# Kernel optimization log

Measured on AMD Instinct MI355X. Metric: run time of the kernel, lower is better.

## Reference

```python
import jax, jax.numpy as jnp
import numpy as np

T, B, XD, H, F = 1024, 256, 64, 256, 256  # seq_len, batch, x_dim, dim_RNN, feature dims
ALPHAS = [0.001, 0.01, 0.1]


def _alphas_per_unit():
    a = np.sort(np.asarray(ALPHAS, dtype=np.float32))
    assign = np.array([a[i % len(a)] for i in range(H)], dtype=np.float32)
    return jnp.asarray(np.sort(assign))  # [H]


def setup_inputs() -> dict:
    key = jax.random.key(0)
    ks = jax.random.split(key, 16)

    def w(k, shape, fan_in):
        return jax.random.normal(k, shape, jnp.float32) / np.sqrt(fan_in).astype(np.float32)

    return {
        "x": jax.random.normal(ks[0], (T, B, XD), jnp.float32),
        # feature_extractor_x: Linear(XD->F), Linear(F->F), tanh after each
        "Wx0": w(ks[1], (F, XD), XD), "bx0": jnp.zeros((F,), jnp.float32),
        "Wx1": w(ks[2], (F, F), F),   "bx1": jnp.zeros((F,), jnp.float32),
        # nn.RNN(F, H): tanh cell
        "Wih": w(ks[3], (H, F), F), "Whh": w(ks[4], (H, H), H),
        "bih": jnp.zeros((H,), jnp.float32), "bhh": jnp.zeros((H,), jnp.float32),
        # mlp_h_x: Linear(H->F), Linear(F->F), tanh after each
        "Wh0": w(ks[5], (F, H), H), "bh0": jnp.zeros((F,), jnp.float32),
        "Wh1": w(ks[6], (F, F), F), "bh1": jnp.zeros((F,), jnp.float32),
        # gen_out: Linear(F->XD)
        "Wg": w(ks[7], (XD, F), F), "bg": jnp.zeros((XD,), jnp.float32),
    }


def reference(x, Wx0, bx0, Wx1, bx1, Wih, Whh, bih, bhh, Wh0, bh0, Wh1, bh1, Wg, bg):
    act = jnp.tanh
    alphas = _alphas_per_unit()  # [H]

    # feature extractor applied to all timesteps at once (non-autonomous path)
    feat = act(jnp.einsum('tbx,fx->tbf', x, Wx0) + bx0)
    feat = act(jnp.einsum('tbf,gf->tbg', feat, Wx1) + bx1)  # [T,B,F]

    def step(h, ft):
        # y_t is generated from h BEFORE the recurrence update
        d = act(h @ Wh0.T + bh0)
        d = act(d @ Wh1.T + bh1)
        y = d @ Wg.T + bg  # [B,XD]
        h_raw = jnp.tanh(ft @ Wih.T + bih + h @ Whh.T + bhh)
        h_new = (1.0 - alphas) * h + alphas * h_raw  # leaky alpha-blend
        return h_new, y

    h0 = jnp.zeros((B, H), x.dtype)
    _, y = jax.lax.scan(step, h0, feat)  # y: [T,B,XD]
    return y
```

## Files before the change

### kernel.cpp

```cpp
#include <hip/hip_runtime.h>
#include <cstddef>


typedef _Float16 halfx8 __attribute__((ext_vector_type(8)));
typedef _Float16 halfx4 __attribute__((ext_vector_type(4)));
typedef float    f32x4  __attribute__((ext_vector_type(4)));

#define T_LEN 1024
#define B_SZ  256
#define H_DIM 256
#define M_ROWS (T_LEN * B_SZ)

__device__ __forceinline__ float fast_tanh(float x) {
  float e = __expf(2.0f * x);
  return 1.0f - 2.0f / (e + 1.0f);
}

__device__ __forceinline__ float alpha_of(int j) {
  return (j < 86) ? 0.001f : ((j < 171) ? 0.01f : 0.1f);
}

__device__ __forceinline__ void lds_barrier() {
  asm volatile("s_waitcnt lgkmcnt(0)\n\ts_barrier" ::: "memory");
}

template <int KCH, bool TANH, bool INF32, bool ZXT>
__global__ __launch_bounds__(512, 2)
void gemm8(const void* __restrict__ Ap, const float* __restrict__ W,
           const float* __restrict__ bias, void* __restrict__ Cp, int mtiles) {
  constexpr int K  = KCH * 32;
  constexpr int KP = K + 8;
  __shared__ __attribute__((aligned(16))) _Float16 Ah[32][KP];

  const int tid  = threadIdx.x;
  const int lane = tid & 63;
  const int wave = tid >> 6;
  const int l15  = lane & 15;
  const int quad = lane >> 4;
  const int jw   = wave * 32;

  halfx8 Bf[2][KCH];
  float  bcol[2];
  int    jj[2];
#pragma unroll
  for (int nt = 0; nt < 2; nt++) {
    jj[nt]   = jw + nt * 16 + l15;
    bcol[nt] = bias[jj[nt]];
#pragma unroll
    for (int ks = 0; ks < KCH; ks++) {
      const float* wp = W + (size_t)jj[nt] * K + ks * 32 + quad * 8;
      float4 w0 = *(const float4*)wp;
      float4 w1 = *(const float4*)(wp + 4);
      halfx8 f;
      f[0] = (_Float16)w0.x; f[1] = (_Float16)w0.y;
      f[2] = (_Float16)w0.z; f[3] = (_Float16)w0.w;
      f[4] = (_Float16)w1.x; f[5] = (_Float16)w1.y;
      f[6] = (_Float16)w1.z; f[7] = (_Float16)w1.w;
      Bf[nt][ks] = f;
    }
  }

  const int srow = tid >> 4;
  const int sk4  = tid & 15;

  for (int bm = blockIdx.x; bm < mtiles; bm += gridDim.x) {
    if constexpr (INF32) {
      const float* A = (const float*)Ap + (size_t)bm * 32 * K;
      constexpr int SEG = K / 64;
      float4 tv[SEG];
#pragma unroll
      for (int s = 0; s < SEG; s++)
        tv[s] = *(const float4*)(A + (size_t)srow * K + (sk4 + s * 16) * 4);
#pragma unroll
      for (int s = 0; s < SEG; s++) {
        halfx4 h;
        h[0] = (_Float16)tv[s].x; h[1] = (_Float16)tv[s].y;
        h[2] = (_Float16)tv[s].z; h[3] = (_Float16)tv[s].w;
        *(halfx4*)&Ah[srow][(sk4 + s * 16) * 4] = h;
      }
    } else {
      const _Float16* A = (const _Float16*)Ap + (size_t)bm * 32 * K;
      constexpr int SEG = K / 128;
      halfx8 tv[SEG];
#pragma unroll
      for (int s = 0; s < SEG; s++)
        tv[s] = *(const halfx8*)(A + (size_t)srow * K + (sk4 + s * 16) * 8);
#pragma unroll
      for (int s = 0; s < SEG; s++)
        *(halfx8*)&Ah[srow][(sk4 + s * 16) * 8] = tv[s];
    }
    lds_barrier();

    f32x4 acc[2][2];
#pragma unroll
    for (int mi = 0; mi < 2; mi++)
#pragma unroll
      for (int nt = 0; nt < 2; nt++) acc[mi][nt] = (f32x4){0.f, 0.f, 0.f, 0.f};

#pragma unroll
    for (int ks = 0; ks < KCH; ks++)
#pragma unroll
      for (int mi = 0; mi < 2; mi++) {
        halfx8 a = *(const halfx8*)&Ah[mi * 16 + l15][ks * 32 + quad * 8];
#pragma unroll
        for (int nt = 0; nt < 2; nt++)
          acc[mi][nt] = __builtin_amdgcn_mfma_f32_16x16x32_f16(a, Bf[nt][ks], acc[mi][nt], 0, 0, 0);
      }

    if constexpr (ZXT) {
      _Float16* C = (_Float16*)Cp;
      const size_t tb = (size_t)(bm >> 3) * (H_DIM * B_SZ) + (bm & 7) * 32 + quad * 4;
#pragma unroll
      for (int mi = 0; mi < 2; mi++)
#pragma unroll
        for (int nt = 0; nt < 2; nt++) {
          halfx4 o;
#pragma unroll
          for (int rg = 0; rg < 4; rg++)
            o[rg] = (_Float16)(acc[mi][nt][rg] + bcol[nt]);
          *(halfx4*)(C + tb + (size_t)jj[nt] * B_SZ + mi * 16) = o;
        }
    } else {
      _Float16* C = (_Float16*)Cp;
#pragma unroll
      for (int mi = 0; mi < 2; mi++)
#pragma unroll
        for (int nt = 0; nt < 2; nt++)
#pragma unroll
          for (int rg = 0; rg < 4; rg++) {
            const int rowg = bm * 32 + mi * 16 + quad * 4 + rg;
            float v = acc[mi][nt][rg] + bcol[nt];
            if (TANH) v = fast_tanh(v);
            C[(size_t)rowg * 256 + jj[nt]] = (_Float16)v;
          }
    }
    lds_barrier();
  }
}

__global__ __launch_bounds__(256, 2)
void gemm4_out(const _Float16* __restrict__ A, const float* __restrict__ W,
               const float* __restrict__ bias, float* __restrict__ C,
               int mtiles) {
  constexpr int K = 256, KCH = 8, KP = 264;
  __shared__ __attribute__((aligned(16))) _Float16 Ah[32][KP];

  const int tid  = threadIdx.x;
  const int lane = tid & 63;
  const int wave = tid >> 6;
  const int l15  = lane & 15;
  const int quad = lane >> 4;
  const int jcol = wave * 16 + l15;

  halfx8 Bf[KCH];
  const float bc = bias[jcol];
#pragma unroll
  for (int ks = 0; ks < KCH; ks++) {
    const float* wp = W + (size_t)jcol * K + ks * 32 + quad * 8;
    float4 w0 = *(const float4*)wp;
    float4 w1 = *(const float4*)(wp + 4);
    halfx8 f;
    f[0] = (_Float16)w0.x; f[1] = (_Float16)w0.y;
    f[2] = (_Float16)w0.z; f[3] = (_Float16)w0.w;
    f[4] = (_Float16)w1.x; f[5] = (_Float16)w1.y;
    f[6] = (_Float16)w1.z; f[7] = (_Float16)w1.w;
    Bf[ks] = f;
  }

  const int srow = tid >> 3;
  const int sk   = tid & 7;

  for (int bm = blockIdx.x; bm < mtiles; bm += gridDim.x) {
    const _Float16* Ab = A + (size_t)bm * 32 * K;
    halfx8 tv[4];
#pragma unroll
    for (int s = 0; s < 4; s++)
      tv[s] = *(const halfx8*)(Ab + (size_t)srow * K + (sk + s * 8) * 8);
#pragma unroll
    for (int s = 0; s < 4; s++)
      *(halfx8*)&Ah[srow][(sk + s * 8) * 8] = tv[s];
    lds_barrier();

    f32x4 acc[2];
#pragma unroll
    for (int mi = 0; mi < 2; mi++) acc[mi] = (f32x4){0.f, 0.f, 0.f, 0.f};
#pragma unroll
    for (int ks = 0; ks < KCH; ks++)
#pragma unroll
      for (int mi = 0; mi < 2; mi++) {
        halfx8 a = *(const halfx8*)&Ah[mi * 16 + l15][ks * 32 + quad * 8];
        acc[mi] = __builtin_amdgcn_mfma_f32_16x16x32_f16(a, Bf[ks], acc[mi], 0, 0, 0);
      }

#pragma unroll
    for (int mi = 0; mi < 2; mi++)
#pragma unroll
      for (int rg = 0; rg < 4; rg++) {
        const int rowg = bm * 32 + mi * 16 + quad * 4 + rg;
        C[(size_t)rowg * 64 + jcol] = acc[mi][rg] + bc;
      }
    lds_barrier();
  }
}

__global__ __launch_bounds__(1024, 4)
void rnn_serial(const _Float16* __restrict__ zxT,
                _Float16* __restrict__ h_all,
                const float* __restrict__ Whh,
                const float* __restrict__ bhh_p)
{
  __shared__ __attribute__((aligned(16))) _Float16 hB[2][16][264];

  const int tid  = threadIdx.x;
  const int lane = tid & 63;
  const int wave = tid >> 6;
  const int l15  = lane & 15;
  const int quad = lane >> 4;
  const int r0   = blockIdx.x * 16;
  const int jcol = wave * 16 + l15;

  halfx8 Bf[8];
#pragma unroll
  for (int ks = 0; ks < 8; ks++) {
    const float* wp = Whh + (size_t)jcol * H_DIM + ks * 32 + quad * 8;
    float4 w0 = *(const float4*)wp;
    float4 w1 = *(const float4*)(wp + 4);
    halfx8 f;
    f[0] = (_Float16)w0.x; f[1] = (_Float16)w0.y;
    f[2] = (_Float16)w0.z; f[3] = (_Float16)w0.w;
    f[4] = (_Float16)w1.x; f[5] = (_Float16)w1.y;
    f[6] = (_Float16)w1.z; f[7] = (_Float16)w1.w;
    Bf[ks] = f;
  }
  const float bj  = bhh_p[jcol];
  const float aj  = alpha_of(jcol);
  const float oma = 1.0f - aj;

  for (int i = tid; i < 16 * 264; i += 1024) (&hB[0][0][0])[i] = (_Float16)0.0f;
  __syncthreads();

  const _Float16* rdp[2] = {&hB[0][l15][quad * 8], &hB[1][l15][quad * 8]};
  _Float16*       wrp[2] = {&hB[1][quad * 4][jcol], &hB[0][quad * 4][jcol]};

  const _Float16* zp = zxT + (size_t)jcol * B_SZ + r0 + quad * 4;
  _Float16*       hp = h_all + (size_t)(r0 + quad * 4) * H_DIM + jcol;
  constexpr int STRIDE = B_SZ * H_DIM;

  float  zc[4];
  halfx4 zA;
  {
    halfx4 z0 = *(const halfx4*)zp;
    zA = *(const halfx4*)(zp + STRIDE);
    zp += 2 * (size_t)STRIDE;
#pragma unroll
    for (int rg = 0; rg < 4; rg++) zc[rg] = (float)z0[rg];
  }

  float    hreg[4] = {0.f, 0.f, 0.f, 0.f};
  _Float16 hh[4]   = {(_Float16)0.f, (_Float16)0.f, (_Float16)0.f, (_Float16)0.f};

  auto step = [&](int p) {
    halfx4 znew = *(const halfx4*)zp;
    zp += STRIDE;

    f32x4 acc = {0.f, 0.f, 0.f, 0.f};
    const _Float16* rd = rdp[p];
#pragma unroll
    for (int ks = 0; ks < 8; ks++) {
      halfx8 a = *(const halfx8*)(rd + ks * 32);
      acc = __builtin_amdgcn_mfma_f32_16x16x32_f16(a, Bf[ks], acc, 0, 0, 0);
    }

    _Float16* wr = wrp[p];
#pragma unroll
    for (int rg = 0; rg < 4; rg++) {
      float ho = hreg[rg];
      float hr = fast_tanh(zc[rg] + acc[rg] + bj);
      float hn = oma * ho + aj * hr;
      hp[rg * H_DIM] = hh[rg];
      hreg[rg] = hn;
      _Float16 hf = (_Float16)hn;
      hh[rg] = hf;
      wr[rg * 264] = hf;
    }
    hp += STRIDE;

    lds_barrier();

#pragma unroll
    for (int rg = 0; rg < 4; rg++) zc[rg] = (float)zA[rg];
    zA = znew;
  };

  for (int it = 0; it < T_LEN / 2; ++it) {
    step(0);
    step(1);
  }
}

extern "C" void kernel_launch(void* const* d_in, const int* in_sizes, int n_in,
                              void* d_out, int out_size, void* d_ws, size_t ws_size,
                              hipStream_t stream) {
  const float* x   = (const float*)d_in[0];
  const float* Wx0 = (const float*)d_in[1];
  const float* bx0 = (const float*)d_in[2];
  const float* Wx1 = (const float*)d_in[3];
  const float* bx1 = (const float*)d_in[4];
  const float* Wih = (const float*)d_in[5];
  const float* Whh = (const float*)d_in[6];
  const float* bih = (const float*)d_in[7];
  const float* bhh = (const float*)d_in[8];
  const float* Wh0 = (const float*)d_in[9];
  const float* bh0 = (const float*)d_in[10];
  const float* Wh1 = (const float*)d_in[11];
  const float* bh1 = (const float*)d_in[12];
  const float* Wg  = (const float*)d_in[13];
  const float* bg  = (const float*)d_in[14];
  float* out = (float*)d_out;

  _Float16* bufA = (_Float16*)d_ws;
  _Float16* bufB = bufA + (size_t)M_ROWS * 256;

  const int MT = M_ROWS / 32;

  gemm8<2, true, true, false><<<512, 512, 0, stream>>>(x, Wx0, bx0, bufA, MT);
  gemm8<8, true, false, false><<<512, 512, 0, stream>>>(bufA, Wx1, bx1, bufB, MT);
  gemm8<8, false, false, true><<<512, 512, 0, stream>>>(bufB, Wih, bih, bufA, MT);
  rnn_serial<<<16, 1024, 0, stream>>>(bufA, bufB, Whh, bhh);
  gemm8<8, true, false, false><<<512, 512, 0, stream>>>(bufB, Wh0, bh0, bufA, MT);
  gemm8<8, true, false, false><<<512, 512, 0, stream>>>(bufA, Wh1, bh1, bufB, MT);
  gemm4_out<<<512, 256, 0, stream>>>(bufB, Wg, bg, out, MT);
}
```

Measured before the change: 1.466 ms.

## Restructure serial RNN kernel to 4 waves each computing 64 hidden units

The recurrent kernel drops from 16 waves per block to 4. Each wave now holds a 64x256 slice of Whh as the MFMA A operand and runs four 16x16 output tiles per step, reusing the h fragments loaded from LDS across all four tiles. The precomputed input projection is now written in row-major layout instead of transposed, which allows vectorized halfx4 loads of z and stores of h. Fewer waves make the per-step barrier cheaper and cut redundant LDS reads, but each wave now does a longer serial chain of MFMAs per step, and the 128 A-fragment VGPRs per lane raise register pressure.

```diff
diff --git a/kernel.cpp b/kernel.cpp
--- a/kernel.cpp
+++ b/kernel.cpp
@@ -203,8 +203,8 @@
   }
 }
 
-__global__ __launch_bounds__(1024, 4)
-void rnn_serial(const _Float16* __restrict__ zxT,
+__global__ __launch_bounds__(256, 1)
+void rnn_serial(const _Float16* __restrict__ zx,
                 _Float16* __restrict__ h_all,
                 const float* __restrict__ Whh,
                 const float* __restrict__ bhh_p)
@@ -217,79 +217,116 @@
   const int l15  = lane & 15;
   const int quad = lane >> 4;
   const int r0   = blockIdx.x * 16;
-  const int jcol = wave * 16 + l15;
-
-  halfx8 Bf[8];
-#pragma unroll
-  for (int ks = 0; ks < 8; ks++) {
-    const float* wp = Whh + (size_t)jcol * H_DIM + ks * 32 + quad * 8;
-    float4 w0 = *(const float4*)wp;
-    float4 w1 = *(const float4*)(wp + 4);
-    halfx8 f;
-    f[0] = (_Float16)w0.x; f[1] = (_Float16)w0.y;
-    f[2] = (_Float16)w0.z; f[3] = (_Float16)w0.w;
-    f[4] = (_Float16)w1.x; f[5] = (_Float16)w1.y;
-    f[6] = (_Float16)w1.z; f[7] = (_Float16)w1.w;
-    Bf[ks] = f;
-  }
-  const float bj  = bhh_p[jcol];
-  const float aj  = alpha_of(jcol);
-  const float oma = 1.0f - aj;
-
-  for (int i = tid; i < 16 * 264; i += 1024) (&hB[0][0][0])[i] = (_Float16)0.0f;
+  const int jb   = wave * 64;
+
+  halfx8 Af[4][8];
+#pragma unroll
+  for (int mt = 0; mt < 4; mt++) {
+    const int j = jb + mt * 16 + l15;
+#pragma unroll
+    for (int ks = 0; ks < 8; ks++) {
+      const float* wp = Whh + (size_t)j * H_DIM + ks * 32 + quad * 8;
+      float4 w0 = *(const float4*)wp;
+      float4 w1 = *(const float4*)(wp + 4);
+      halfx8 f;
+      f[0] = (_Float16)w0.x; f[1] = (_Float16)w0.y;
+      f[2] = (_Float16)w0.z; f[3] = (_Float16)w0.w;
+      f[4] = (_Float16)w1.x; f[5] = (_Float16)w1.y;
+      f[6] = (_Float16)w1.z; f[7] = (_Float16)w1.w;
+      Af[mt][ks] = f;
+    }
+  }
+
+  float bj[4][4], aj[4][4], oma[4][4];
+#pragma unroll
+  for (int mt = 0; mt < 4; mt++)
+#pragma unroll
+    for (int rg = 0; rg < 4; rg++) {
+      const int j = jb + mt * 16 + quad * 4 + rg;
+      bj[mt][rg]  = bhh_p[j];
+      aj[mt][rg]  = alpha_of(j);
+      oma[mt][rg] = 1.0f - aj[mt][rg];
+    }
+
+  for (int i = tid; i < 16 * 264; i += 256) (&hB[0][0][0])[i] = (_Float16)0.0f;
   __syncthreads();
 
   const _Float16* rdp[2] = {&hB[0][l15][quad * 8], &hB[1][l15][quad * 8]};
-  _Float16*       wrp[2] = {&hB[1][quad * 4][jcol], &hB[0][quad * 4][jcol]};
-
-  const _Float16* zp = zxT + (size_t)jcol * B_SZ + r0 + quad * 4;
-  _Float16*       hp = h_all + (size_t)(r0 + quad * 4) * H_DIM + jcol;
+  _Float16*       wrp[2] = {&hB[1][l15][jb + quad * 4], &hB[0][l15][jb + quad * 4]};
+
   constexpr int STRIDE = B_SZ * H_DIM;
-
-  float  zc[4];
-  halfx4 zA;
+  const _Float16* zp = zx    + (size_t)(r0 + l15) * H_DIM + jb + quad * 4;
+  _Float16*       hp = h_all + (size_t)(r0 + l15) * H_DIM + jb + quad * 4;
+
+  float  zc[4][4];
+  halfx4 zA[4];
   {
-    halfx4 z0 = *(const halfx4*)zp;
-    zA = *(const halfx4*)(zp + STRIDE);
+#pragma unroll
+    for (int mt = 0; mt < 4; mt++) {
+      halfx4 z0 = *(const halfx4*)(zp + mt * 16);
+      zA[mt]    = *(const halfx4*)(zp + mt * 16 + STRIDE);
+#pragma unroll
+      for (int rg = 0; rg < 4; rg++) zc[mt][rg] = (float)z0[rg];
+    }
     zp += 2 * (size_t)STRIDE;
-#pragma unroll
-    for (int rg = 0; rg < 4; rg++) zc[rg] = (float)z0[rg];
-  }
-
-  float    hreg[4] = {0.f, 0.f, 0.f, 0.f};
-  _Float16 hh[4]   = {(_Float16)0.f, (_Float16)0.f, (_Float16)0.f, (_Float16)0.f};
+  }
+
+  float  hreg[4][4];
+  halfx4 hh4[4];
+#pragma unroll
+  for (int mt = 0; mt < 4; mt++) {
+#pragma unroll
+    for (int rg = 0; rg < 4; rg++) {
+      hreg[mt][rg] = 0.0f;
+      hh4[mt][rg]  = (_Float16)0.0f;
+    }
+  }
 
   auto step = [&](int p) {
-    halfx4 znew = *(const halfx4*)zp;
+    halfx4 znew[4];
+#pragma unroll
+    for (int mt = 0; mt < 4; mt++) znew[mt] = *(const halfx4*)(zp + mt * 16);
     zp += STRIDE;
 
-    f32x4 acc = {0.f, 0.f, 0.f, 0.f};
     const _Float16* rd = rdp[p];
-#pragma unroll
-    for (int ks = 0; ks < 8; ks++) {
-      halfx8 a = *(const halfx8*)(rd + ks * 32);
-      acc = __builtin_amdgcn_mfma_f32_16x16x32_f16(a, Bf[ks], acc, 0, 0, 0);
-    }
+    halfx8 hb[8];
+#pragma unroll
+    for (int ks = 0; ks < 8; ks++) hb[ks] = *(const halfx8*)(rd + ks * 32);
+
+    f32x4 acc[4];
+#pragma unroll
+    for (int mt = 0; mt < 4; mt++) acc[mt] = (f32x4){0.f, 0.f, 0.f, 0.f};
+#pragma unroll
+    for (int ks = 0; ks < 8; ks++)
+#pragma unroll
+      for (int mt = 0; mt < 4; mt++)
+        acc[mt] = __builtin_amdgcn_mfma_f32_16x16x32_f16(Af[mt][ks], hb[ks], acc[mt], 0, 0, 0);
 
     _Float16* wr = wrp[p];
 #pragma unroll
-    for (int rg = 0; rg < 4; rg++) {
-      float ho = hreg[rg];
-      float hr = fast_tanh(zc[rg] + acc[rg] + bj);
-      float hn = oma * ho + aj * hr;
-      hp[rg * H_DIM] = hh[rg];
-      hreg[rg] = hn;
-      _Float16 hf = (_Float16)hn;
-      hh[rg] = hf;
-      wr[rg * 264] = hf;
+    for (int mt = 0; mt < 4; mt++) {
+      halfx4 hnew;
+#pragma unroll
+      for (int rg = 0; rg < 4; rg++) {
+        float hr = fast_tanh(zc[mt][rg] + acc[mt][rg] + bj[mt][rg]);
+        float hn = oma[mt][rg] * hreg[mt][rg] + aj[mt][rg] * hr;
+        hreg[mt][rg] = hn;
+        hnew[rg] = (_Float16)hn;
+      }
+      *(halfx4*)(hp + mt * 16) = hh4[mt];
+      hh4[mt] = hnew;
+      *(halfx4*)(wr + mt * 16) = hnew;
     }
     hp += STRIDE;
 
     lds_barrier();
 
 #pragma unroll
-    for (int rg = 0; rg < 4; rg++) zc[rg] = (float)zA[rg];
-    zA = znew;
+    for (int mt = 0; mt < 4; mt++) {
+#pragma unroll
+      for (int rg = 0; rg < 4; rg++) zc[mt][rg] = (float)zA[mt][rg];
+      zA[mt] = znew[mt];
+    }
   };
 
   for (int it = 0; it < T_LEN / 2; ++it) {
@@ -325,8 +362,8 @@
 
   gemm8<2, true, true, false><<<512, 512, 0, stream>>>(x, Wx0, bx0, bufA, MT);
   gemm8<8, true, false, false><<<512, 512, 0, stream>>>(bufA, Wx1, bx1, bufB, MT);
-  gemm8<8, false, false, true><<<512, 512, 0, stream>>>(bufB, Wih, bih, bufA, MT);
-  rnn_serial<<<16, 1024, 0, stream>>>(bufA, bufB, Whh, bhh);
+  gemm8<8, false, false, false><<<512, 512, 0, stream>>>(bufB, Wih, bih, bufA, MT);
+  rnn_serial<<<16, 256, 0, stream>>>(bufA, bufB, Whh, bhh);
   gemm8<8, true, false, false><<<512, 512, 0, stream>>>(bufB, Wh0, bh0, bufA, MT);
   gemm8<8, true, false, false><<<512, 512, 0, stream>>>(bufA, Wh1, bh1, bufB, MT);
   gemm4_out<<<512, 256, 0, stream>>>(bufB, Wg, bg, out, MT);
```

New measurement: 1.727 ms. +17.8%, slower.
